# Kernel optimization log

Hardware: AMD Instinct MI355X
Metric: run time of the kernel (lower is better)

## Reference

```python
import jax, jax.numpy as jnp
import numpy as np

C = 4096
N = 16384


def setup_inputs() -> dict:
    key = jax.random.key(0)
    k1, k2, k3 = jax.random.split(key, 3)
    x = jax.random.normal(k1, (N, C), dtype=jnp.float32)
    # fc params, torch default init: U(-1/sqrt(C), 1/sqrt(C))
    bound = 1.0 / np.sqrt(C)
    W = jax.random.uniform(k2, (C, C), dtype=jnp.float32, minval=-bound, maxval=bound)
    b = jax.random.uniform(k3, (C,), dtype=jnp.float32, minval=-bound, maxval=bound)
    return {"x": x, "W": W, "b": b, "scale_factor": 2}


def reference(x, W, b, scale_factor):
    # MyGAP_fc: mean over batch -> [1, C] (kept as [C])
    x_gap = jnp.mean(x, axis=0)                      # [C]
    # fc: torch Linear y = x @ W.T + b
    x_scale = x_gap @ W.T + b                        # [C]
    x_scale = jax.nn.sigmoid(x_scale * scale_factor) # [C]
    # training-mode path (no hard thresholding)
    # MyScale_fc: per-channel broadcast multiply
    x_out = x * x_scale[None, :]                     # [N, C]
    return (x_out, x_scale)
```

## Files before the change

kernel.cpp:

```cpp
#include <hip/hip_runtime.h>

#define C 4096
#define NROWS 16384
#define NBLK 256
#define TPB 1024
#define RPB 64
#define HWREG_XCC_ID 63508

typedef float f32x4 __attribute__((ext_vector_type(4)));

__device__ __forceinline__ unsigned aload(unsigned* p) {
    return __hip_atomic_load(p, __ATOMIC_RELAXED, __HIP_MEMORY_SCOPE_AGENT);
}
__device__ __forceinline__ unsigned aadd(unsigned* p, unsigned v) {
    return __hip_atomic_fetch_add(p, v, __ATOMIC_RELAXED, __HIP_MEMORY_SCOPE_AGENT);
}

#define CTRL_WORDS 2048

__device__ __forceinline__ void gbar(unsigned* ctrl, unsigned r, bool& lead,
                                     unsigned xcd) {
    __syncthreads();
    if (threadIdx.x == 0) {
        unsigned tkt = aadd(&ctrl[64 * xcd], 1u);
        if (r == 1 && tkt == 0) {
            lead = true;
            unsigned lv = aadd(&ctrl[640], 1u);
            asm volatile("" :: "v"(lv));
        }
        if (lead) {
            for (;;) {
                unsigned s = 0;
#pragma unroll
                for (int i = 0; i < 8; ++i) s += aload(&ctrl[64 * i]);
                if (s >= r * NBLK) break;
                __builtin_amdgcn_s_sleep(2);
            }
            unsigned v = __hip_atomic_fetch_add(&ctrl[576], 0u, __ATOMIC_ACQ_REL,
                                                __HIP_MEMORY_SCOPE_AGENT);
            asm volatile("" :: "v"(v));
            aadd(&ctrl[704], 1u);
            while (aload(&ctrl[704]) < r * aload(&ctrl[640]))
                __builtin_amdgcn_s_sleep(2);
            __hip_atomic_store(&ctrl[1024 + 64 * xcd], r, __ATOMIC_RELAXED,
                               __HIP_MEMORY_SCOPE_AGENT);
        } else {
            while (aload(&ctrl[1024 + 64 * xcd]) < r) __builtin_amdgcn_s_sleep(8);
        }
    }
    __syncthreads();
}

__global__ __launch_bounds__(TPB, 4)
void fused_kernel(const float* __restrict__ x, const float* __restrict__ W,
                  const float* __restrict__ b, const int* __restrict__ sf,
                  float* __restrict__ out, float* __restrict__ ws) {
    float* part = ws;
    float* gsum = ws + (size_t)NBLK * C;
    unsigned* ctrl = (unsigned*)(gsum + C);

    __shared__ float lds[TPB];

    const int t = threadIdx.x;
    const int bidx = blockIdx.x;
    const int r0 = bidx * RPB;
    const float sf0 = (float)sf[0];
    const unsigned xcd = __builtin_amdgcn_s_getreg(HWREG_XCC_ID) & 7u;
    bool lead = false;

    {
        const f32x4* xv = (const f32x4*)x + (size_t)r0 * (C / 4) + t;
        f32x4 acc = {0.f, 0.f, 0.f, 0.f};
#pragma unroll 8
        for (int r = 0; r < RPB; ++r)
            acc += xv[(size_t)r * (C / 4)];
        __builtin_nontemporal_store(acc, (f32x4*)part + (size_t)bidx * (C / 4) + t);
    }
    gbar(ctrl, 1, lead, xcd);

    {
        const int col = (bidx << 4) + (t & 15);
        const int rg = t >> 4;
        float s = 0.f;
#pragma unroll
        for (int i = 0; i < 4; ++i)
            s += part[(size_t)(rg * 4 + i) * C + col];
        lds[t] = s;
        __syncthreads();
#pragma unroll
        for (int h = 32; h >= 1; h >>= 1) {
            if (rg < h) lds[t] += lds[t + h * 16];
            __syncthreads();
        }
        if (t < 16) gsum[(bidx << 4) + t] = lds[t];
    }
    gbar(ctrl, 2, lead, xcd);

    {
        const int wave = t >> 6, lane = t & 63;
        const int row = (bidx << 4) + wave;
        const f32x4* wv = (const f32x4*)(W + (size_t)row * C);
        const f32x4* gv = (const f32x4*)gsum;
        float acc = 0.f;
#pragma unroll
        for (int i = 0; i < 16; ++i) {
            const f32x4 w4 = __builtin_nontemporal_load(wv + (i << 6) + lane);
            const f32x4 g4 = gv[(i << 6) + lane];
            acc += w4.x * g4.x + w4.y * g4.y + w4.z * g4.z + w4.w * g4.w;
        }
#pragma unroll
        for (int off = 32; off; off >>= 1) acc += __shfl_down(acc, off);
        if (lane == 0) {
            const float y = acc * (1.0f / NROWS) + b[row];
            out[(size_t)NROWS * C + row] = 1.0f / (1.0f + __expf(-sf0 * y));
        }
    }
    gbar(ctrl, 3, lead, xcd);

    {
        const f32x4 sc = ((const f32x4*)(out + (size_t)NROWS * C))[t];
        const f32x4* xv = (const f32x4*)x + (size_t)r0 * (C / 4) + t;
        f32x4* ov = (f32x4*)out + (size_t)r0 * (C / 4) + t;
#pragma unroll 8
        for (int r = 0; r < RPB; ++r) {
            f32x4 v = xv[(size_t)r * (C / 4)];
            v *= sc;
            __builtin_nontemporal_store(v, ov + (size_t)r * (C / 4));
        }
    }
}

extern "C" void kernel_launch(void* const* d_in, const int* in_sizes, int n_in,
                              void* d_out, int out_size, void* d_ws, size_t ws_size,
                              hipStream_t stream) {
    const float* x = (const float*)d_in[0];
    const float* W = (const float*)d_in[1];
    const float* b = (const float*)d_in[2];
    const int* sf  = (const int*)d_in[3];

    float* out = (float*)d_out;
    float* ws  = (float*)d_ws;

    const size_t ctrl_off = ((size_t)NBLK * C + C) * sizeof(float);
    hipMemsetAsync((char*)d_ws + ctrl_off, 0, CTRL_WORDS * sizeof(unsigned), stream);

    fused_kernel<<<NBLK, TPB, 0, stream>>>(x, W, b, sf, out, ws);
}
```

Before: 182.1 us.

## Replace partial-sum buffer with per-XCD atomic accumulation and drop one grid barrier

Column partial sums are now accumulated with float atomicAdd into eight per-XCD slices instead of each block writing its own row of a 256-row partials buffer. After the first grid barrier, every block sums the eight slices into LDS and computes its GEMV rows from there, which removes the separate reduction phase and one grid-wide barrier. The barrier control words are reorganised so the per-XCD arrival counters are separate from the leader election counters. The cost is about a million float atomics landing on a small region, a memset that is now larger, and summation order that is no longer deterministic.

```diff
diff --git a/kernel.cpp b/kernel.cpp
--- a/kernel.cpp
+++ b/kernel.cpp
@@ -22,12 +22,14 @@
                                      unsigned xcd) {
     __syncthreads();
     if (threadIdx.x == 0) {
-        unsigned tkt = aadd(&ctrl[64 * xcd], 1u);
-        if (r == 1 && tkt == 0) {
-            lead = true;
-            unsigned lv = aadd(&ctrl[640], 1u);
-            asm volatile("" :: "v"(lv));
+        if (r == 1) {
+            if (aadd(&ctrl[512 + 64 * xcd], 1u) == 0) {
+                lead = true;
+                unsigned lv = aadd(&ctrl[1088], 1u);
+                asm volatile("" :: "v"(lv) : "memory");
+            }
         }
+        aadd(&ctrl[64 * xcd], 1u);
         if (lead) {
             for (;;) {
                 unsigned s = 0;
@@ -36,16 +38,16 @@
                 if (s >= r * NBLK) break;
                 __builtin_amdgcn_s_sleep(2);
             }
-            unsigned v = __hip_atomic_fetch_add(&ctrl[576], 0u, __ATOMIC_ACQ_REL,
+            unsigned v = __hip_atomic_fetch_add(&ctrl[1024], 0u, __ATOMIC_ACQ_REL,
                                                 __HIP_MEMORY_SCOPE_AGENT);
-            asm volatile("" :: "v"(v));
-            aadd(&ctrl[704], 1u);
-            while (aload(&ctrl[704]) < r * aload(&ctrl[640]))
+            asm volatile("" :: "v"(v) : "memory");
+            aadd(&ctrl[1152], 1u);
+            while (aload(&ctrl[1152]) < r * aload(&ctrl[1088]))
                 __builtin_amdgcn_s_sleep(2);
-            __hip_atomic_store(&ctrl[1024 + 64 * xcd], r, __ATOMIC_RELAXED,
+            __hip_atomic_store(&ctrl[1280 + 64 * xcd], r, __ATOMIC_RELAXED,
                                __HIP_MEMORY_SCOPE_AGENT);
         } else {
-            while (aload(&ctrl[1024 + 64 * xcd]) < r) __builtin_amdgcn_s_sleep(8);
+            while (aload(&ctrl[1280 + 64 * xcd]) < r) __builtin_amdgcn_s_sleep(8);
         }
     }
     __syncthreads();
@@ -55,11 +57,10 @@
 void fused_kernel(const float* __restrict__ x, const float* __restrict__ W,
                   const float* __restrict__ b, const int* __restrict__ sf,
                   float* __restrict__ out, float* __restrict__ ws) {
-    float* part = ws;
-    float* gsum = ws + (size_t)NBLK * C;
-    unsigned* ctrl = (unsigned*)(gsum + C);
+    float* gsumX = ws;
+    unsigned* ctrl = (unsigned*)(ws + 8 * (size_t)C);
 
-    __shared__ float lds[TPB];
+    __shared__ float g_lds[C];
 
     const int t = threadIdx.x;
     const int bidx = blockIdx.x;
@@ -74,33 +75,27 @@
 #pragma unroll 8
         for (int r = 0; r < RPB; ++r)
             acc += xv[(size_t)r * (C / 4)];
-        __builtin_nontemporal_store(acc, (f32x4*)part + (size_t)bidx * (C / 4) + t);
+        float* g = gsumX + (size_t)xcd * C + t * 4;
+        atomicAdd(g + 0, acc.x);
+        atomicAdd(g + 1, acc.y);
+        atomicAdd(g + 2, acc.z);
+        atomicAdd(g + 3, acc.w);
     }
     gbar(ctrl, 1, lead, xcd);
 
     {
-        const int col = (bidx << 4) + (t & 15);
-        const int rg = t >> 4;
-        float s = 0.f;
+        f32x4 s = {0.f, 0.f, 0.f, 0.f};
 #pragma unroll
-        for (int i = 0; i < 4; ++i)
-            s += part[(size_t)(rg * 4 + i) * C + col];
-        lds[t] = s;
-        __syncthreads();
-#pragma unroll
-        for (int h = 32; h >= 1; h >>= 1) {
-            if (rg < h) lds[t] += lds[t + h * 16];
-            __syncthreads();
-        }
-        if (t < 16) gsum[(bidx << 4) + t] = lds[t];
+        for (int xx = 0; xx < 8; ++xx)
+            s += ((const f32x4*)(gsumX + (size_t)xx * C))[t];
+        ((f32x4*)g_lds)[t] = s;
     }
-    gbar(ctrl, 2, lead, xcd);
-
+    __syncthreads();
     {
         const int wave = t >> 6, lane = t & 63;
         const int row = (bidx << 4) + wave;
         const f32x4* wv = (const f32x4*)(W + (size_t)row * C);
-        const f32x4* gv = (const f32x4*)gsum;
+        const f32x4* gv = (const f32x4*)g_lds;
         float acc = 0.f;
 #pragma unroll
         for (int i = 0; i < 16; ++i) {
@@ -115,7 +110,7 @@
             out[(size_t)NROWS * C + row] = 1.0f / (1.0f + __expf(-sf0 * y));
         }
     }
-    gbar(ctrl, 3, lead, xcd);
+    gbar(ctrl, 2, lead, xcd);
 
     {
         const f32x4 sc = ((const f32x4*)(out + (size_t)NROWS * C))[t];
@@ -141,8 +136,8 @@
     float* out = (float*)d_out;
     float* ws  = (float*)d_ws;
 
-    const size_t ctrl_off = ((size_t)NBLK * C + C) * sizeof(float);
-    hipMemsetAsync((char*)d_ws + ctrl_off, 0, CTRL_WORDS * sizeof(unsigned), stream);
+    hipMemsetAsync(d_ws, 0, (8 * (size_t)C) * sizeof(float)
+                            + CTRL_WORDS * sizeof(unsigned), stream);
 
     fused_kernel<<<NBLK, TPB, 0, stream>>>(x, W, b, sf, out, ws);
 }
```

Measured after the change: 180.7 us. Within noise of the previous version (-0.7%).
